# Performance work log

Hardware: AMD Instinct MI355X
Metric: run time of the kernel (lower is better)

## Reference

```python
import jax, jax.numpy as jnp
import numpy as np

NUM_HEAD = 8
DIM_HEAD = 32
IN_DIM = 256  # = NUM_HEAD * DIM_HEAD
SLEN = 1024
BSZ = 8


def setup_inputs() -> dict:
    key = jax.random.key(0)
    ks = jax.random.split(key, 6)
    std = 1.0 / np.sqrt(DIM_HEAD).astype(np.float32)
    h = jax.random.normal(ks[0], (SLEN, BSZ, IN_DIM), dtype=jnp.float32)
    W_y = std * jax.random.normal(ks[1], (1, NUM_HEAD, DIM_HEAD, DIM_HEAD), dtype=jnp.float32)
    W_q = std * jax.random.normal(ks[2], (1, NUM_HEAD, DIM_HEAD, DIM_HEAD), dtype=jnp.float32)
    W_k = std * jax.random.normal(ks[3], (1, NUM_HEAD, DIM_HEAD, DIM_HEAD), dtype=jnp.float32)
    w_b = std * jax.random.normal(ks[4], (1, NUM_HEAD, DIM_HEAD, 4), dtype=jnp.float32)
    # out_linear: Linear(H*d -> in_dim, bias=False); torch weight shape (in_dim, H*d)
    W_out = jax.random.normal(ks[5], (IN_DIM, NUM_HEAD * DIM_HEAD), dtype=jnp.float32) / np.sqrt(NUM_HEAD * DIM_HEAD).astype(np.float32)
    return {"h": h, "W_y": W_y, "W_q": W_q, "W_k": W_k, "w_b": w_b, "W_out": W_out}


def _read(W, v):
    # W: (B,H,d,d), v: (B,H,d) -> (B,H,d)
    return jnp.einsum('bhij,bhj->bhi', W, v)


def _read_b(wb, v):
    # wb: (B,H,d,4), v: (B,H,d) -> (B,H,4)
    return jnp.einsum('bhik,bhi->bhk', wb, v)


def _srwm_forward(h, W_y, W_q, W_k, w_b, W_out):
    slen, bsz, _ = h.shape
    # reshape to heads and softmax the input (as in the torch forward)
    x = jax.nn.softmax(h.reshape(slen, bsz, NUM_HEAD, DIM_HEAD), axis=-1)  # (S,B,H,d)
    bc = lambda W: jnp.broadcast_to(W, (bsz,) + W.shape[1:])
    carry0 = (bc(W_y), bc(W_q), bc(W_k), bc(w_b))

    def step(carry, xt):
        Wy, Wq, Wk, wb = carry  # (B,H,d,d) x3, (B,H,d,4)
        yt = _read(Wy, xt)                                   # output read with current Wy
        qt = jax.nn.softmax(_read(Wq, xt), axis=-1)          # query
        kt = jax.nn.softmax(_read(Wk, xt), axis=-1)          # key
        bt = jax.nn.sigmoid(_read_b(wb, xt))                 # (B,H,4) learning rates
        # delta-rule self-referential update: W += beta * (W q - W k) (x) k
        dy = _read(Wy, qt) - _read(Wy, kt)
        dq = _read(Wq, qt) - _read(Wq, kt)
        dk = _read(Wk, qt) - _read(Wk, kt)
        db = _read_b(wb, qt) - _read_b(wb, kt)               # (B,H,4)
        outer = lambda u: u[..., :, None] * kt[..., None, :]
        Wy = Wy + bt[..., 0][..., None, None] * outer(dy)
        Wq = Wq + bt[..., 1][..., None, None] * outer(dq)
        Wk = Wk + bt[..., 2][..., None, None] * outer(dk)
        wb = wb + bt[..., 3][..., None, None] * (kt[..., :, None] * db[..., None, :])
        return (Wy, Wq, Wk, wb), yt

    _, ys = jax.lax.scan(step, carry0, x)                    # ys: (S,B,H,d)
    out = ys.reshape(slen, bsz, NUM_HEAD * DIM_HEAD) @ W_out.T  # (S,B,in_dim)
    return h + out  # dropout p=0 -> identity; residual


def reference(h, W_y, W_q, W_k, w_b, W_out):
    return _srwm_forward(h, W_y, W_q, W_k, w_b, W_out)
```

## Files before the change

### kernel.cpp

```cpp
#include <hip/hip_runtime.h>

#define DEV __device__ __forceinline__

typedef float f2 __attribute__((ext_vector_type(2)));


DEV f2 pkfma(f2 a, f2 b, f2 c) {
  asm("v_pk_fma_f32 %0, %1, %2, %0" : "+v"(c) : "v"(a), "v"(b));
  return c;
}
DEV f2 pkfma3(f2 a, f2 b, f2 c) {
  f2 d;
  asm("v_pk_fma_f32 %0, %1, %2, %3" : "=v"(d) : "v"(a), "v"(b), "v"(c));
  return d;
}
DEV f2 pkadd(f2 a, f2 b) {
  f2 d;
  asm("v_pk_add_f32 %0, %1, %2" : "=v"(d) : "v"(a), "v"(b));
  return d;
}


template <int CTRL>
DEV float dppf(float x) {
  return __int_as_float(__builtin_amdgcn_update_dpp(
      0, __float_as_int(x), CTRL, 0xF, 0xF, true));
}

DEV float wsum32(float v) {
  v += dppf<0xB1>(v);
  v += dppf<0x4E>(v);
  v += dppf<0x141>(v);
  v += dppf<0x140>(v);
#if __has_builtin(__builtin_amdgcn_permlane16_swap)
  {
    auto p = __builtin_amdgcn_permlane16_swap(
        __float_as_uint(v), __float_as_uint(v), false, false);
    v = __uint_as_float(p[0]) + __uint_as_float(p[1]);
  }
#else
  v += __shfl_xor(v, 16, 64);
#endif
  return v;
}

DEV float halfsum(float v) {
#if __has_builtin(__builtin_amdgcn_permlane32_swap)
  auto p = __builtin_amdgcn_permlane32_swap(
      __float_as_uint(v), __float_as_uint(v), false, false);
  return __uint_as_float(p[0]) + __uint_as_float(p[1]);
#else
  return v + __shfl_xor(v, 32, 64);
#endif
}

#define SLEN 1024
#define NH 8
#define DH 32
#define HSTRIDE 2048


__global__ __launch_bounds__(256)
void srwm_xsm(const float* __restrict__ h, float* __restrict__ x) {
  int i = blockIdx.x * 256 + threadIdx.x;
  float e = __expf(h[i]);
  x[i] = __fdividef(e, wsum32(e));
}


#define BARRIER()                                        \
  do {                                                   \
    __builtin_amdgcn_sched_barrier(0);                   \
    asm volatile("s_waitcnt lgkmcnt(0)");                \
    __builtin_amdgcn_sched_barrier(0);                   \
    __builtin_amdgcn_s_barrier();                        \
    __builtin_amdgcn_sched_barrier(0);                   \
  } while (0)

#define LDX4(DST, PTR)                                                        \
  { _Pragma("unroll") for (int i_ = 0; i_ < 4; ++i_) {                        \
      float4 a_ = *(const float4*)((PTR) + 4 * i_);                           \
      DST[2*i_]   = f2{a_.x, a_.y};                                           \
      DST[2*i_+1] = f2{a_.z, a_.w}; } }

#define REGION(P, QV, KV, BP, QN, KN, BPN, XS, XP, XPF, YPTR)                 \
  {                                                                           \
                                          \
    f2 dv[8];                                                                 \
    _Pragma("unroll") for (int j = 0; j < 8; ++j)                             \
      dv[j] = pkfma3(KV[j], mone, QV[j]);                          \
    f2 daA={0.f,0.f}, daB={0.f,0.f}, dbA={0.f,0.f}, dbB={0.f,0.f};            \
    f2 sA={0.f,0.f}, sB={0.f,0.f};                                            \
    _Pragma("unroll") for (int j = 0; j < 8; j += 2) {                        \
      daA = pkfma(Wa2[j],   dv[j],   daA);                                    \
      daB = pkfma(Wa2[j+1], dv[j+1], daB);                                    \
      dbA = pkfma(Wb2[j],   dv[j],   dbA);                                    \
      dbB = pkfma(Wb2[j+1], dv[j+1], dbB);                                    \
      sA  = pkfma(KV[j],    XS[j],   sA);                                     \
      sB  = pkfma(KV[j+1],  XS[j+1], sB);                                     \
    }                                                                         \
    f2 dac = pkadd(daA, daB), dbc = pkadd(dbA, dbB), sc = pkadd(sA, sB);      \
    float da = halfsum(dac.x + dac.y);                                        \
    float db = halfsum(dbc.x + dbc.y);                                        \
    float sv = halfsum(sc.x + sc.y);                                          \
    float ua = BP.x * da, ub = BP.y * db;                                     \
    float aA = fmaf(ua, sv, preAa);                                           \
    float aB = fmaf(ub, sv, preAb);                                           \
    if (w == 0) {                                                             \
      if (lane < DH) *(YPTR) = aA;                                   \
      float e = __expf(aB);                                                   \
      shb[(P)*72 + r] = __fdividef(e, wsum32(e));                    \
    } else {                                                                  \
      float e = __expf(aA);                                                   \
      shb[(P)*72 + 32 + r] = __fdividef(e, wsum32(e));               \
      float sg = __fdividef(1.f, 1.f + __expf(-aB));                          \
      if (lane < 4) shb[(P)*72 + 64 + lane] = sg;                    \
    }                                                                         \
    BARRIER();                                                                \
                                   \
    LDX4(QN, &shb[(P)*72 + c0]);                                              \
    LDX4(KN, &shb[(P)*72 + 32 + c0]);                                         \
    BPN = *(const float2*)&shb[(P)*72 + 64 + 2*w];                            \
    f2 uua = f2{ua, ua}, uub = f2{ub, ub};                                    \
    _Pragma("unroll") for (int j = 0; j < 8; ++j) {                           \
      Wa2[j] = pkfma(uua, KV[j], Wa2[j]);                                     \
      Wb2[j] = pkfma(uub, KV[j], Wb2[j]);                                     \
    }                                                                         \
    LDX4(XS, XPF);                                      \
    f2 paA={0.f,0.f}, paB={0.f,0.f}, pbA={0.f,0.f}, pbB={0.f,0.f};            \
    _Pragma("unroll") for (int j = 0; j < 8; j += 2) {                        \
      paA = pkfma(Wa2[j],   XP[j],   paA);                                    \
      paB = pkfma(Wa2[j+1], XP[j+1], paB);                                    \
      pbA = pkfma(Wb2[j],   XP[j],   pbA);                                    \
      pbB = pkfma(Wb2[j+1], XP[j+1], pbB);                                    \
    }                                                                         \
    f2 pac = pkadd(paA, paB), pbc = pkadd(pbA, pbB);                          \
    preAa = halfsum(pac.x + pac.y);                                           \
    preAb = halfsum(pbc.x + pbc.y);                                           \
  }

__global__ __launch_bounds__(128, 1)
void srwm_scan(const float* __restrict__ Wy0, const float* __restrict__ Wq0,
               const float* __restrict__ Wk0, const float* __restrict__ wb0,
               float* xy) {
  __align__(16) __shared__ float shb[2 * 72];

  const int bh   = blockIdx.x;
  const int hd   = bh & 7;
  const int w    = threadIdx.x >> 6;
  const int lane = threadIdx.x & 63;
  const int r    = lane & 31;
  const int c0   = (lane >> 5) * 16;

  const f2 mone = f2{-1.f, -1.f};

  f2 Wa2[8], Wb2[8];
  if (w == 0) {
    const float* pa = Wy0 + (hd * DH + r) * DH + c0;
    const float* pb = Wq0 + (hd * DH + r) * DH + c0;
    LDX4(Wa2, pa);
    LDX4(Wb2, pb);
  } else {
    const float* pa = Wk0 + (hd * DH + r) * DH + c0;
    LDX4(Wa2, pa);
    const int kk = r & 3;
#pragma unroll
    for (int j = 0; j < 8; ++j)
      Wb2[j] = f2{wb0[(hd * DH + c0 + 2*j) * 4 + kk],
                  wb0[(hd * DH + c0 + 2*j + 1) * 4 + kk]};
  }

  float* xb = xy + bh * DH;

  f2 X0[8], X1[8];
  LDX4(X0, xb + c0);
  LDX4(X1, xb + HSTRIDE + c0);

  float preAa, preAb;
  {
    f2 paA={0.f,0.f}, paB={0.f,0.f}, pbA={0.f,0.f}, pbB={0.f,0.f};
#pragma unroll
    for (int j = 0; j < 8; j += 2) {
      paA = pkfma(Wa2[j],   X0[j],   paA);
      paB = pkfma(Wa2[j+1], X0[j+1], paB);
      pbA = pkfma(Wb2[j],   X0[j],   pbA);
      pbB = pkfma(Wb2[j+1], X0[j+1], pbB);
    }
    f2 pac = pkadd(paA, paB), pbc = pkadd(pbA, pbB);
    preAa = halfsum(pac.x + pac.y);
    preAb = halfsum(pbc.x + pbc.y);
  }

  f2 QA[8], KA[8], QB[8], KB[8];
  const f2 z2 = f2{0.f, 0.f};
#pragma unroll
  for (int j = 0; j < 8; ++j) { QA[j] = z2; KA[j] = z2; }
  float2 BPA = {0.f, 0.f}, BPB = {0.f, 0.f};

  __syncthreads();

  const float* xpf = xb + 2 * HSTRIDE + c0;
  float*       yst = xb + lane;

  for (int t = 0; t < SLEN - 4; t += 2) {
    REGION(0, QA, KA, BPA, QB, KB, BPB, X0, X1, xpf,           yst);
    REGION(1, QB, KB, BPB, QA, KA, BPA, X1, X0, xpf + HSTRIDE, yst + HSTRIDE);
    xpf += 2 * HSTRIDE;
    yst += 2 * HSTRIDE;
  }
  {
    const float* xlast = xb + (size_t)(SLEN - 1) * HSTRIDE + c0;
    REGION(0, QA, KA, BPA, QB, KB, BPB, X0, X1, xlast - HSTRIDE, yst);
    REGION(1, QB, KB, BPB, QA, KA, BPA, X1, X0, xlast,           yst + HSTRIDE);
    yst += 2 * HSTRIDE;
    REGION(0, QA, KA, BPA, QB, KB, BPB, X0, X1, xlast, yst);
    REGION(1, QB, KB, BPB, QA, KA, BPA, X1, X0, xlast, yst + HSTRIDE);
  }
}


__global__ __launch_bounds__(256)
void srwm_proj(const float* __restrict__ h, const float* __restrict__ ys,
               const float* __restrict__ Wout, float* __restrict__ out) {
  __shared__ float ytile[32][256];
  const int r0  = blockIdx.x * 32;
  const int tid = threadIdx.x;

  const float4* src = (const float4*)(ys + (size_t)r0 * 256);
  float4*       dst = (float4*)(&ytile[0][0]);
#pragma unroll
  for (int i = 0; i < 8; ++i) dst[tid + i * 256] = src[tid + i * 256];
  __syncthreads();

  float acc[32];
#pragma unroll
  for (int m = 0; m < 32; ++m) acc[m] = 0.f;

  const float* wrow = Wout + (size_t)tid * 256;
  for (int k = 0; k < 256; k += 4) {
    float4 wv = *(const float4*)(wrow + k);
#pragma unroll
    for (int m = 0; m < 32; ++m) {
      float4 y4 = *(const float4*)(&ytile[m][k]);
      acc[m] = fmaf(wv.x, y4.x,
               fmaf(wv.y, y4.y,
               fmaf(wv.z, y4.z,
               fmaf(wv.w, y4.w, acc[m]))));
    }
  }

#pragma unroll
  for (int m = 0; m < 32; ++m) {
    int row = r0 + m;
    out[(size_t)row * 256 + tid] = h[(size_t)row * 256 + tid] + acc[m];
  }
}


extern "C" void kernel_launch(void* const* d_in, const int* in_sizes, int n_in,
                              void* d_out, int out_size, void* d_ws, size_t ws_size,
                              hipStream_t stream) {
  const float* h    = (const float*)d_in[0];
  const float* Wy0  = (const float*)d_in[1];
  const float* Wq0  = (const float*)d_in[2];
  const float* Wk0  = (const float*)d_in[3];
  const float* wb0  = (const float*)d_in[4];
  const float* Wout = (const float*)d_in[5];
  float* out = (float*)d_out;

  srwm_xsm <<<SLEN * HSTRIDE / 256, 256, 0, stream>>>(h, out);
  srwm_scan<<<64, 128, 0, stream>>>(Wy0, Wq0, Wk0, wb0, out);
  srwm_proj<<<256, 256, 0, stream>>>(h, out, Wout, out);
}
```

Baseline: 526.9 us.

## Defer softmax normalization and sigmoid past the barrier to shorten the serial critical path

Writers now store unnormalized exp values and the raw beta pre-activation to shared memory. Readers recompute the softmax sums and the sigmoid after the barrier. The 1/sum scales are folded into the delta, score and update coefficients. This removes the cross-lane wsum32 reduction and the divide from the path before the barrier, and moves the W update ahead of the barrier. The cost is redundant sum and sigmoid work per thread, and initial Q/K values of one with a 1/32 scale.

```diff
diff --git a/kernel.cpp b/kernel.cpp
--- a/kernel.cpp
+++ b/kernel.cpp
@@ -17,6 +17,11 @@
 DEV f2 pkadd(f2 a, f2 b) {
   f2 d;
   asm("v_pk_add_f32 %0, %1, %2" : "=v"(d) : "v"(a), "v"(b));
+  return d;
+}
+DEV f2 pkmul(f2 a, f2 b) {
+  f2 d;
+  asm("v_pk_mul_f32 %0, %1, %2" : "=v"(d) : "v"(a), "v"(b));
   return d;
 }
 
@@ -83,12 +88,13 @@
       DST[2*i_]   = f2{a_.x, a_.y};                                           \
       DST[2*i_+1] = f2{a_.z, a_.w}; } }
 
-#define REGION(P, QV, KV, BP, QN, KN, BPN, XS, XP, XPF, YPTR)                 \
+#define REGION(P, QV, KV, BP, RQ, RK, QN, KN, BPN, RQN, RKN, XS, XP, XPF, YPTR) \
   {                                                                           \
-                                          \
+                   \
+    f2 rqv = f2{RQ, RQ}, mrkv = f2{-RK, -RK};                                 \
     f2 dv[8];                                                                 \
     _Pragma("unroll") for (int j = 0; j < 8; ++j)                             \
-      dv[j] = pkfma3(KV[j], mone, QV[j]);                          \
+      dv[j] = pkfma3(QV[j], rqv, pkmul(KV[j], mrkv));              \
     f2 daA={0.f,0.f}, daB={0.f,0.f}, dbA={0.f,0.f}, dbB={0.f,0.f};            \
     f2 sA={0.f,0.f}, sB={0.f,0.f};                                            \
     _Pragma("unroll") for (int j = 0; j < 8; j += 2) {                        \
@@ -102,30 +108,38 @@
     f2 dac = pkadd(daA, daB), dbc = pkadd(dbA, dbB), sc = pkadd(sA, sB);      \
     float da = halfsum(dac.x + dac.y);                                        \
     float db = halfsum(dbc.x + dbc.y);                                        \
-    float sv = halfsum(sc.x + sc.y);                                          \
+    float sv = halfsum(sc.x + sc.y) * RK;                \
     float ua = BP.x * da, ub = BP.y * db;                                     \
     float aA = fmaf(ua, sv, preAa);                                           \
     float aB = fmaf(ub, sv, preAb);                                           \
+                           \
     if (w == 0) {                                                             \
       if (lane < DH) *(YPTR) = aA;                                   \
-      float e = __expf(aB);                                                   \
-      shb[(P)*72 + r] = __fdividef(e, wsum32(e));                    \
+      shb[(P)*72 + r] = __expf(aB);                             \
     } else {                                                                  \
-      float e = __expf(aA);                                                   \
-      shb[(P)*72 + 32 + r] = __fdividef(e, wsum32(e));               \
-      float sg = __fdividef(1.f, 1.f + __expf(-aB));                          \
-      if (lane < 4) shb[(P)*72 + 64 + lane] = sg;                    \
-    }                                                                         \
-    BARRIER();                                                                \
-                                   \
-    LDX4(QN, &shb[(P)*72 + c0]);                                              \
-    LDX4(KN, &shb[(P)*72 + 32 + c0]);                                         \
-    BPN = *(const float2*)&shb[(P)*72 + 64 + 2*w];                            \
-    f2 uua = f2{ua, ua}, uub = f2{ub, ub};                                    \
+      shb[(P)*72 + 32 + r] = __expf(aA);                        \
+      if (lane < 4) shb[(P)*72 + 64 + lane] = aB;        \
+    }                                                                         \
+       \
+    float uaK = ua * RK, ubK = ub * RK;                                       \
+    f2 uua = f2{uaK, uaK}, uub = f2{ubK, ubK};                                \
     _Pragma("unroll") for (int j = 0; j < 8; ++j) {                           \
       Wa2[j] = pkfma(uua, KV[j], Wa2[j]);                                     \
       Wb2[j] = pkfma(uub, KV[j], Wb2[j]);                                     \
     }                                                                         \
+    BARRIER();                                                                \
+                    \
+    LDX4(QN, &shb[(P)*72 + c0]);                                              \
+    LDX4(KN, &shb[(P)*72 + 32 + c0]);                                         \
+    float2 braw = *(const float2*)&shb[(P)*72 + 64 + 2*w];                    \
+    { f2 sq = QN[0], sk = KN[0];                                              \
+      _Pragma("unroll") for (int j = 1; j < 8; ++j) {                         \
+        sq = pkadd(sq, QN[j]); sk = pkadd(sk, KN[j]);                         \
+      }                                                                       \
+      RQN = __fdividef(1.f, halfsum(sq.x + sq.y));                            \
+      RKN = __fdividef(1.f, halfsum(sk.x + sk.y)); }                          \
+    BPN.x = __fdividef(1.f, 1.f + __expf(-braw.x));                           \
+    BPN.y = __fdividef(1.f, 1.f + __expf(-braw.y));                           \
     LDX4(XS, XPF);                                      \
     f2 paA={0.f,0.f}, paB={0.f,0.f}, pbA={0.f,0.f}, pbB={0.f,0.f};            \
     _Pragma("unroll") for (int j = 0; j < 8; j += 2) {                        \
@@ -151,8 +165,6 @@
   const int lane = threadIdx.x & 63;
   const int r    = lane & 31;
   const int c0   = (lane >> 5) * 16;
-
-  const f2 mone = f2{-1.f, -1.f};
 
   f2 Wa2[8], Wb2[8];
   if (w == 0) {
@@ -192,10 +204,11 @@
   }
 
   f2 QA[8], KA[8], QB[8], KB[8];
-  const f2 z2 = f2{0.f, 0.f};
-#pragma unroll
-  for (int j = 0; j < 8; ++j) { QA[j] = z2; KA[j] = z2; }
+  const f2 one2 = f2{1.f, 1.f};
+#pragma unroll
+  for (int j = 0; j < 8; ++j) { QA[j] = one2; KA[j] = one2; }
   float2 BPA = {0.f, 0.f}, BPB = {0.f, 0.f};
+  float rqA = 1.f / 32.f, rkA = 1.f / 32.f, rqB = 1.f / 32.f, rkB = 1.f / 32.f;
 
   __syncthreads();
 
@@ -203,18 +216,24 @@
   float*       yst = xb + lane;
 
   for (int t = 0; t < SLEN - 4; t += 2) {
-    REGION(0, QA, KA, BPA, QB, KB, BPB, X0, X1, xpf,           yst);
-    REGION(1, QB, KB, BPB, QA, KA, BPA, X1, X0, xpf + HSTRIDE, yst + HSTRIDE);
+    REGION(0, QA, KA, BPA, rqA, rkA, QB, KB, BPB, rqB, rkB,
+           X0, X1, xpf, yst);
+    REGION(1, QB, KB, BPB, rqB, rkB, QA, KA, BPA, rqA, rkA,
+           X1, X0, xpf + HSTRIDE, yst + HSTRIDE);
     xpf += 2 * HSTRIDE;
     yst += 2 * HSTRIDE;
   }
   {
     const float* xlast = xb + (size_t)(SLEN - 1) * HSTRIDE + c0;
-    REGION(0, QA, KA, BPA, QB, KB, BPB, X0, X1, xlast - HSTRIDE, yst);
-    REGION(1, QB, KB, BPB, QA, KA, BPA, X1, X0, xlast,           yst + HSTRIDE);
+    REGION(0, QA, KA, BPA, rqA, rkA, QB, KB, BPB, rqB, rkB,
+           X0, X1, xlast - HSTRIDE, yst);
+    REGION(1, QB, KB, BPB, rqB, rkB, QA, KA, BPA, rqA, rkA,
+           X1, X0, xlast, yst + HSTRIDE);
     yst += 2 * HSTRIDE;
-    REGION(0, QA, KA, BPA, QB, KB, BPB, X0, X1, xlast, yst);
-    REGION(1, QB, KB, BPB, QA, KA, BPA, X1, X0, xlast, yst + HSTRIDE);
+    REGION(0, QA, KA, BPA, rqA, rkA, QB, KB, BPB, rqB, rkB,
+           X0, X1, xlast, yst);
+    REGION(1, QB, KB, BPB, rqB, rkB, QA, KA, BPA, rqA, rkA,
+           X1, X0, xlast, yst + HSTRIDE);
   }
 }
 
```

New measurement: 637.4 us. 1.21x slower.
